# Performance work log

Measured on AMD Instinct MI355X. Metric: run time of the kernel, lower is better.

The kernel has to match this reference:

```python
import jax, jax.numpy as jnp
import numpy as np

N_NODES = 50000
N_EDGES = 800000
IN_CH, HID_CH, OUT_CH = 128, 128, 40


def setup_inputs() -> dict:
    key = jax.random.key(0)
    k1, k2, k3, k4 = jax.random.split(key, 4)
    x = jax.random.normal(k1, (N_NODES, IN_CH), dtype=jnp.float32)
    edge_index = jax.random.randint(k2, (2, N_EDGES), 0, N_NODES, dtype=jnp.int64)
    # Glorot-ish init for linear weights
    W1 = jax.random.normal(k3, (IN_CH, HID_CH), dtype=jnp.float32) / np.sqrt(IN_CH)
    b1 = jnp.zeros((HID_CH,), dtype=jnp.float32)
    W2 = jax.random.normal(k4, (HID_CH, OUT_CH), dtype=jnp.float32) / np.sqrt(HID_CH)
    b2 = jnp.zeros((OUT_CH,), dtype=jnp.float32)
    return {"x": x, "edge_index": edge_index, "W1": W1, "b1": b1, "W2": W2, "b2": b2}


def _gcn_conv(x, src, dst, W, b):
    # GCNConv(normalize=False): dense transform then sparse aggregation (scatter-add)
    h = x @ W                                   # [N, C_out]
    out = jax.ops.segment_sum(h[src], dst, num_segments=N_NODES)  # sum_{j->i} h[j]
    return out + b


def reference(x, edge_index, W1, b1, W2, b2):
    src, dst = edge_index[0], edge_index[1]
    h = _gcn_conv(x, src, dst, W1, b1)
    h = jax.nn.relu(h)
    # dropout is identity in eval mode
    h = _gcn_conv(h, src, dst, W2, b2)
    return jax.nn.log_softmax(h, axis=-1)
```

## Files before the change

kernel.cpp:

```cpp
#include <hip/hip_runtime.h>

#define NN 50000
#define NE 800000
#define NBKT 196
#define NBLK 256
#define EPB (NE / NBLK)
#define MATN (NBKT * NBLK)

using short8 = __attribute__((ext_vector_type(8))) short;
using f32x4  = __attribute__((ext_vector_type(4))) float;
union U4S8 { uint4 u; short8 v; };

__device__ __forceinline__ float lof(unsigned v) { return __uint_as_float(v << 16); }
__device__ __forceinline__ float hif(unsigned v) { return __uint_as_float(v & 0xffff0000u); }
__device__ __forceinline__ unsigned bf16rne(float f) {
    unsigned u = __float_as_uint(f);
    return (u + 0x7fffu + ((u >> 16) & 1u)) >> 16;
}
__device__ __forceinline__ unsigned pack2(float a, float b) {
    return bf16rne(a) | (bf16rne(b) << 16);
}
__device__ __forceinline__ unsigned fp8pack4(float a0, float a1, float a2, float a3) {
    int w = __builtin_amdgcn_cvt_pk_fp8_f32(a0, a1, 0, false);
    w = __builtin_amdgcn_cvt_pk_fp8_f32(a2, a3, w, true);
    return (unsigned)w;
}

__global__ __launch_bounds__(256) void binhist_k(const int* __restrict__ dst,
                                                 int* __restrict__ mat,
                                                 const float* __restrict__ W1,
                                                 const float* __restrict__ W2,
                                                 unsigned* __restrict__ W1T,
                                                 unsigned* __restrict__ W2T) {
    __shared__ int hist[NBKT];
    const int tid = threadIdx.x;
    for (int i = tid; i < NBKT; i += 256) hist[i] = 0;

    const int g = blockIdx.x * 256 + tid;
    if (g < 8192) {
        const int n = g >> 6, k2 = (g & 63) * 2;
        W1T[g] = pack2(W1[k2 * 128 + n], W1[(k2 + 1) * 128 + n]);
    } else if (g < 8192 + 3072) {
        const int u = g - 8192;
        const int n = u >> 6;
        const int q0 = (u & 63) * 2, q1 = q0 + 1;
        const int c0 = (q0 & 7) * 16 + (q0 >> 3);
        const int c1 = (q1 & 7) * 16 + (q1 >> 3);
        W2T[u] = (n < 40) ? pack2(W2[c0 * 40 + n], W2[c1 * 40 + n]) : 0u;
    }
    __syncthreads();

    const int base = blockIdx.x * EPB;
    for (int e = base + tid; e < base + EPB; e += 256)
        atomicAdd(&hist[dst[e] >> 8], 1);
    __syncthreads();
    for (int i = tid; i < NBKT; i += 256)
        mat[i * NBLK + blockIdx.x] = hist[i];
}

__global__ __launch_bounds__(256) void reduce_k(const int* __restrict__ mat,
                                                int* __restrict__ blocksum) {
    int v = mat[blockIdx.x * NBLK + threadIdx.x];
#pragma unroll
    for (int off = 32; off; off >>= 1) v += __shfl_xor(v, off, 64);
    __shared__ int ws[4];
    if ((threadIdx.x & 63) == 0) ws[threadIdx.x >> 6] = v;
    __syncthreads();
    if (threadIdx.x == 0) blocksum[blockIdx.x] = ws[0] + ws[1] + ws[2] + ws[3];
}

__global__ __launch_bounds__(256) void scanfin_k(int* __restrict__ mat,
                                                 const int* __restrict__ blocksum,
                                                 int* __restrict__ bucketoff) {
    __shared__ int bs[256];
    __shared__ int sm[256];
    const int t = threadIdx.x;
    const int b = blockIdx.x;
    const int mybs = (t < NBKT) ? blocksum[t] : 0;
    bs[t] = mybs;
    __syncthreads();
#pragma unroll
    for (int off = 1; off < 256; off <<= 1) {
        int u = (t >= off) ? bs[t - off] : 0;
        __syncthreads();
        bs[t] += u;
        __syncthreads();
    }
    if (b == 0) {
        if (t < NBKT) bucketoff[t] = bs[t] - mybs;
        if (t == 0) bucketoff[NBKT] = NE;
    }
    const int boff = bs[b] - blocksum[b];

    const int v = mat[b * NBLK + t];
    sm[t] = v;
    __syncthreads();
#pragma unroll
    for (int off = 1; off < 256; off <<= 1) {
        int u = (t >= off) ? sm[t - off] : 0;
        __syncthreads();
        sm[t] += u;
        __syncthreads();
    }
    mat[b * NBLK + t] = boff + sm[t] - v;
}

__global__ __launch_bounds__(256) void scatter_k(const int* __restrict__ src,
                                                 const int* __restrict__ dst,
                                                 const int* __restrict__ mat,
                                                 unsigned* __restrict__ binned) {
    __shared__ int cur[NBKT];
    const int tid = threadIdx.x;
    for (int i = tid; i < NBKT; i += 256) cur[i] = mat[i * NBLK + blockIdx.x];
    __syncthreads();
    const int base = blockIdx.x * EPB;
    for (int e = base + tid; e < base + EPB; e += 256) {
        const int d = dst[e];
        const int p = atomicAdd(&cur[d >> 8], 1);
        binned[p] = ((unsigned)(d & 255) << 16) | (unsigned)src[e];
    }
}

__global__ __launch_bounds__(256) void csrgemm1_k(const unsigned* __restrict__ binned,
                                                  const int* __restrict__ bucketoff,
                                                  int* __restrict__ rowoff,
                                                  unsigned short* __restrict__ eid,
                                                  const float* __restrict__ x,
                                                  const unsigned* __restrict__ W1T,
                                                  uint2* __restrict__ H1) {
    __shared__ int cnt[256];
    __shared__ int off[256];
    const int tid = threadIdx.x;
    if (blockIdx.x < NBKT) {
        const int b = blockIdx.x;
        const int beg = bucketoff[b];
        const int end = bucketoff[b + 1];
        cnt[tid] = 0;
        __syncthreads();
        for (int i = beg + tid; i < end; i += 256)
            atomicAdd(&cnt[(binned[i] >> 16) & 255u], 1);
        __syncthreads();
        const int v = cnt[tid];
        off[tid] = v;
        __syncthreads();
#pragma unroll
        for (int o = 1; o < 256; o <<= 1) {
            int u = (tid >= o) ? off[tid - o] : 0;
            __syncthreads();
            off[tid] += u;
            __syncthreads();
        }
        const int excl = off[tid] - v;
        const int node = b * 256 + tid;
        if (node <= NN) rowoff[node] = beg + excl;
        cnt[tid] = excl;
        __syncthreads();
        for (int i = beg + tid; i < end; i += 256) {
            const unsigned e = binned[i];
            const int p = atomicAdd(&cnt[(e >> 16) & 255u], 1);
            eid[beg + p] = (unsigned short)(e & 0xffffu);
        }
        return;
    }
    const int lane = tid & 63;
    const int cl = lane & 15;
    const int kh = lane >> 4;
    const int gw = ((blockIdx.x - NBKT) * 256 + tid) >> 6;

    short8 Bf[8][4];
#pragma unroll
    for (int c = 0; c < 8; ++c)
#pragma unroll
        for (int kc = 0; kc < 4; ++kc) {
            U4S8 tb;
            tb.u = *(const uint4*)(W1T + ((c * 16 + cl) * 128 + kc * 32 + kh * 8) / 2);
            Bf[c][kc] = tb.v;
        }

    for (int mt = gw; mt < 3125; mt += 1024) {
        const int r0 = mt * 16;
        const float* ap = x + (long)(r0 + cl) * 128 + kh * 8;
        f32x4 acc[8];
#pragma unroll
        for (int c = 0; c < 8; ++c) acc[c] = (f32x4){0.f, 0.f, 0.f, 0.f};
#pragma unroll
        for (int kc = 0; kc < 4; ++kc) {
            const float4 p0 = *(const float4*)(ap + kc * 32);
            const float4 p1 = *(const float4*)(ap + kc * 32 + 4);
            U4S8 af;
            af.u.x = pack2(p0.x, p0.y);
            af.u.y = pack2(p0.z, p0.w);
            af.u.z = pack2(p1.x, p1.y);
            af.u.w = pack2(p1.z, p1.w);
#pragma unroll
            for (int c = 0; c < 8; ++c)
                acc[c] = __builtin_amdgcn_mfma_f32_16x16x32_bf16(af.v, Bf[c][kc], acc[c], 0, 0, 0);
        }
#pragma unroll
        for (int j = 0; j < 4; ++j) {
            uint2 o;
            o.x = fp8pack4(acc[0][j], acc[1][j], acc[2][j], acc[3][j]);
            o.y = fp8pack4(acc[4][j], acc[5][j], acc[6][j], acc[7][j]);
            H1[(long)(r0 + kh * 4 + j) * 16 + cl] = o;
        }
    }
}

__global__ __launch_bounds__(256) void gather1_k(const uint4* __restrict__ H1,
                                                 const int* __restrict__ rowoff,
                                                 const unsigned short* __restrict__ eid,
                                                 const float* __restrict__ b1,
                                                 uint4* __restrict__ h) {
    const int n = blockIdx.x * 4 + (threadIdx.x >> 6);
    const int lane = threadIdx.x & 63;
    const int g = lane >> 3;
    const int cl = lane & 7;
    const int beg = rowoff[n], end = rowoff[n + 1];
    float a[16];
#pragma unroll
    for (int i = 0; i < 16; ++i) a[i] = 0.f;

#define ACC16(v)                                                             \
    {                                                                        \
        auto t0 = __builtin_amdgcn_cvt_pk_f32_fp8((int)(v).x, false);        \
        auto t1 = __builtin_amdgcn_cvt_pk_f32_fp8((int)(v).x, true);         \
        auto t2 = __builtin_amdgcn_cvt_pk_f32_fp8((int)(v).y, false);        \
        auto t3 = __builtin_amdgcn_cvt_pk_f32_fp8((int)(v).y, true);         \
        auto t4 = __builtin_amdgcn_cvt_pk_f32_fp8((int)(v).z, false);        \
        auto t5 = __builtin_amdgcn_cvt_pk_f32_fp8((int)(v).z, true);         \
        auto t6 = __builtin_amdgcn_cvt_pk_f32_fp8((int)(v).w, false);        \
        auto t7 = __builtin_amdgcn_cvt_pk_f32_fp8((int)(v).w, true);         \
        a[0] += t0[0];  a[1] += t0[1];  a[2] += t1[0];  a[3] += t1[1];       \
        a[4] += t2[0];  a[5] += t2[1];  a[6] += t3[0];  a[7] += t3[1];       \
        a[8] += t4[0];  a[9] += t4[1];  a[10] += t5[0]; a[11] += t5[1];      \
        a[12] += t6[0]; a[13] += t6[1]; a[14] += t7[0]; a[15] += t7[1];      \
    }

    int k = beg;
    for (; k + 15 < end; k += 16) {
        const uint4 vA = H1[eid[k + g] * 8 + cl];
        const uint4 vB = H1[eid[k + 8 + g] * 8 + cl];
        ACC16(vA);
        ACC16(vB);
    }
    for (; k + 7 < end; k += 8) {
        const uint4 v = H1[eid[k + g] * 8 + cl];
        ACC16(v);
    }
    if (k + g < end) {
        const uint4 v = H1[eid[k + g] * 8 + cl];
        ACC16(v);
    }
#undef ACC16

#pragma unroll
    for (int i = 0; i < 16; ++i) {
        a[i] += __shfl_xor(a[i], 8, 64);
        a[i] += __shfl_xor(a[i], 16, 64);
        a[i] += __shfl_xor(a[i], 32, 64);
    }
    if (lane < 8) {
        float r[16];
#pragma unroll
        for (int i = 0; i < 16; ++i)
            r[i] = fmaxf(a[i] + b1[(i & 7) * 16 + cl * 2 + (i >> 3)], 0.f);
        uint4 o1, o2;
        o1.x = pack2(r[0], r[1]);  o1.y = pack2(r[2], r[3]);
        o1.z = pack2(r[4], r[5]);  o1.w = pack2(r[6], r[7]);
        o2.x = pack2(r[8], r[9]);  o2.y = pack2(r[10], r[11]);
        o2.z = pack2(r[12], r[13]); o2.w = pack2(r[14], r[15]);
        h[n * 16 + cl * 2] = o1;
        h[n * 16 + cl * 2 + 1] = o2;
    }
}

__global__ __launch_bounds__(256) void gemm2_k(const unsigned* __restrict__ h,
                                               const unsigned* __restrict__ W2T,
                                               unsigned short* __restrict__ H2) {
    const int lane = threadIdx.x & 63;
    const int cl = lane & 15;
    const int kh = lane >> 4;
    const int gw = (blockIdx.x * 256 + threadIdx.x) >> 6;

    short8 Bf[3][4];
#pragma unroll
    for (int c = 0; c < 3; ++c)
#pragma unroll
        for (int kc = 0; kc < 4; ++kc) {
            U4S8 tb;
            tb.u = *(const uint4*)(W2T + ((c * 16 + cl) * 128 + kc * 32 + kh * 8) / 2);
            Bf[c][kc] = tb.v;
        }

    for (int mt = gw; mt < 3125; mt += 1024) {
        const int r0 = mt * 16;
        const unsigned* ap = h + (long)(r0 + cl) * 64 + kh * 4;
        f32x4 acc[3];
#pragma unroll
        for (int c = 0; c < 3; ++c) acc[c] = (f32x4){0.f, 0.f, 0.f, 0.f};
#pragma unroll
        for (int kc = 0; kc < 4; ++kc) {
            U4S8 af;
            af.u = *(const uint4*)(ap + kc * 16);
#pragma unroll
            for (int c = 0; c < 3; ++c)
                acc[c] = __builtin_amdgcn_mfma_f32_16x16x32_bf16(af.v, Bf[c][kc], acc[c], 0, 0, 0);
        }
        unsigned short* hp = H2 + (long)(r0 + kh * 4) * 64;
#pragma unroll
        for (int c = 0; c < 3; ++c) {
            const int col = c * 16 + cl;
            if (col < 40) {
#pragma unroll
                for (int j = 0; j < 4; ++j)
                    hp[j * 64 + col] = (unsigned short)bf16rne(acc[c][j]);
            }
        }
    }
}

__global__ __launch_bounds__(256) void gather2_k(const uint2* __restrict__ H2,
                                                 const int* __restrict__ rowoff,
                                                 const unsigned short* __restrict__ eid,
                                                 const float* __restrict__ b2,
                                                 float* __restrict__ out) {
    const int n = blockIdx.x * 4 + (threadIdx.x >> 6);
    const int lane = threadIdx.x & 63;
    const int g = lane / 10;
    const int c2 = lane - g * 10;
    const int beg = rowoff[n], end = rowoff[n + 1];
    float ax = 0.f, ay = 0.f, az = 0.f, aw = 0.f;
    if (g < 6) {
        int k = beg + g;
        for (; k + 6 < end; k += 12) {
            const uint2 v0 = H2[eid[k] * 16 + c2];
            const uint2 v1 = H2[eid[k + 6] * 16 + c2];
            ax += lof(v0.x) + lof(v1.x);
            ay += hif(v0.x) + hif(v1.x);
            az += lof(v0.y) + lof(v1.y);
            aw += hif(v0.y) + hif(v1.y);
        }
        if (k < end) {
            const uint2 v = H2[eid[k] * 16 + c2];
            ax += lof(v.x); ay += hif(v.x);
            az += lof(v.y); aw += hif(v.y);
        }
    }
    ax += __shfl(ax, lane + 30, 64); ay += __shfl(ay, lane + 30, 64);
    az += __shfl(az, lane + 30, 64); aw += __shfl(aw, lane + 30, 64);
    ax += __shfl(ax, lane + 10, 64) + __shfl(ax, lane + 20, 64);
    ay += __shfl(ay, lane + 10, 64) + __shfl(ay, lane + 20, 64);
    az += __shfl(az, lane + 10, 64) + __shfl(az, lane + 20, 64);
    aw += __shfl(aw, lane + 10, 64) + __shfl(aw, lane + 20, 64);

    const bool act = (lane < 10);
    float4 b = {0.f, 0.f, 0.f, 0.f};
    if (act) b = ((const float4*)b2)[lane];
    const float vx = ax + b.x, vy = ay + b.y, vz = az + b.z, vw = aw + b.w;
    float m = act ? fmaxf(fmaxf(vx, vy), fmaxf(vz, vw)) : -INFINITY;
#pragma unroll
    for (int off = 32; off; off >>= 1) m = fmaxf(m, __shfl_xor(m, off, 64));
    float e = act ? (expf(vx - m) + expf(vy - m) + expf(vz - m) + expf(vw - m)) : 0.f;
#pragma unroll
    for (int off = 32; off; off >>= 1) e += __shfl_xor(e, off, 64);
    const float ls = logf(e);
    if (act) {
        float4 o = {vx - m - ls, vy - m - ls, vz - m - ls, vw - m - ls};
        ((float4*)(out + (long)n * 40))[lane] = o;
    }
}

extern "C" void kernel_launch(void* const* d_in, const int* in_sizes, int n_in,
                              void* d_out, int out_size, void* d_ws, size_t ws_size,
                              hipStream_t stream) {
    const float* x  = (const float*)d_in[0];
    const int*   ei = (const int*)d_in[1];
    const float* W1 = (const float*)d_in[2];
    const float* b1 = (const float*)d_in[3];
    const float* W2 = (const float*)d_in[4];
    const float* b2 = (const float*)d_in[5];
    const int* src = ei;
    const int* dst = ei + NE;

    unsigned* H1   = (unsigned*)d_ws;
    unsigned* h    = H1 + (size_t)NN * 32;
    unsigned* H2   = h + (size_t)NN * 64;
    unsigned* W1T  = H2 + (size_t)NN * 32;
    unsigned* W2T  = W1T + 8192;
    int* mat       = (int*)(W2T + 3072);
    int* blocksum  = mat + MATN;
    int* bucketoff = blocksum + 256;
    int* rowoff    = bucketoff + NBKT + 1;
    unsigned short* eid = (unsigned short*)(rowoff + NN + 1);
    unsigned* binned = h;
    float* out     = (float*)d_out;

    binhist_k<<<NBLK, 256, 0, stream>>>(dst, mat, W1, W2, W1T, W2T);
    reduce_k<<<NBKT, 256, 0, stream>>>(mat, blocksum);
    scanfin_k<<<NBKT, 256, 0, stream>>>(mat, blocksum, bucketoff);
    scatter_k<<<NBLK, 256, 0, stream>>>(src, dst, mat, binned);
    csrgemm1_k<<<NBKT + 256, 256, 0, stream>>>(binned, bucketoff, rowoff, eid,
                                               x, W1T, (uint2*)H1);
    gather1_k<<<12500, 256, 0, stream>>>((const uint4*)H1, rowoff, eid, b1, (uint4*)h);
    gemm2_k<<<256, 256, 0, stream>>>(h, W2T, (unsigned short*)H2);
    gather2_k<<<12500, 256, 0, stream>>>((const uint2*)H2, rowoff, eid, b2, out);
}
```

Before: 106.2 us.

## Fuse histogram scan into scatter kernel and widen layer-2 gather loads

```diff
diff --git a/kernel.cpp b/kernel.cpp
--- a/kernel.cpp
+++ b/kernel.cpp
@@ -58,62 +58,53 @@
         mat[i * NBLK + blockIdx.x] = hist[i];
 }
 
-__global__ __launch_bounds__(256) void reduce_k(const int* __restrict__ mat,
-                                                int* __restrict__ blocksum) {
-    int v = mat[blockIdx.x * NBLK + threadIdx.x];
-#pragma unroll
-    for (int off = 32; off; off >>= 1) v += __shfl_xor(v, off, 64);
-    __shared__ int ws[4];
-    if ((threadIdx.x & 63) == 0) ws[threadIdx.x >> 6] = v;
+__global__ __launch_bounds__(256) void scanscatter_k(const int* __restrict__ src,
+                                                     const int* __restrict__ dst,
+                                                     const int* __restrict__ mat,
+                                                     unsigned* __restrict__ binned,
+                                                     int* __restrict__ bucketoff) {
+    __shared__ int tot[NBKT];
+    __shared__ int cur[NBKT];
+    __shared__ int sc[256];
+    const int tid = threadIdx.x;
+    const int lane = tid & 63;
+    const int w = tid >> 6;
+    const int b = blockIdx.x;
+    for (int i = w; i < NBKT; i += 4) {
+        int t = 0, p = 0;
+#pragma unroll
+        for (int c = 0; c < 4; ++c) {
+            const int col = c * 64 + lane;
+            const int v = mat[i * NBLK + col];
+            t += v;
+            p += (col < b) ? v : 0;
+        }
+#pragma unroll
+        for (int off = 32; off; off >>= 1) {
+            t += __shfl_xor(t, off, 64);
+            p += __shfl_xor(p, off, 64);
+        }
+        if (lane == 0) { tot[i] = t; cur[i] = p; }
+    }
     __syncthreads();
-    if (threadIdx.x == 0) blocksum[blockIdx.x] = ws[0] + ws[1] + ws[2] + ws[3];
-}
-
-__global__ __launch_bounds__(256) void scanfin_k(int* __restrict__ mat,
-                                                 const int* __restrict__ blocksum,
-                                                 int* __restrict__ bucketoff) {
-    __shared__ int bs[256];
-    __shared__ int sm[256];
-    const int t = threadIdx.x;
-    const int b = blockIdx.x;
-    const int mybs = (t < NBKT) ? blocksum[t] : 0;
-    bs[t] = mybs;
+    const int v = (tid < NBKT) ? tot[tid] : 0;
+    sc[tid] = v;
     __syncthreads();
 #pragma unroll
     for (int off = 1; off < 256; off <<= 1) {
-        int u = (t >= off) ? bs[t - off] : 0;
-        __syncthreads();
-        bs[t] += u;
-        __syncthreads();
-    }
+        int u = (tid >= off) ? sc[tid - off] : 0;
+        __syncthreads();
+        sc[tid] += u;
+        __syncthreads();
+    }
+    const int excl = sc[tid] - v;
+    if (tid < NBKT) cur[tid] += excl;
     if (b == 0) {
-        if (t < NBKT) bucketoff[t] = bs[t] - mybs;
-        if (t == 0) bucketoff[NBKT] = NE;
-    }
-    const int boff = bs[b] - blocksum[b];
-
-    const int v = mat[b * NBLK + t];
-    sm[t] = v;
+        if (tid < NBKT) bucketoff[tid] = excl;
+        if (tid == 0) bucketoff[NBKT] = NE;
+    }
     __syncthreads();
-#pragma unroll
-    for (int off = 1; off < 256; off <<= 1) {
-        int u = (t >= off) ? sm[t - off] : 0;
-        __syncthreads();
-        sm[t] += u;
-        __syncthreads();
-    }
-    mat[b * NBLK + t] = boff + sm[t] - v;
-}
-
-__global__ __launch_bounds__(256) void scatter_k(const int* __restrict__ src,
-                                                 const int* __restrict__ dst,
-                                                 const int* __restrict__ mat,
-                                                 unsigned* __restrict__ binned) {
-    __shared__ int cur[NBKT];
-    const int tid = threadIdx.x;
-    for (int i = tid; i < NBKT; i += 256) cur[i] = mat[i * NBLK + blockIdx.x];
-    __syncthreads();
-    const int base = blockIdx.x * EPB;
+    const int base = b * EPB;
     for (int e = base + tid; e < base + EPB; e += 256) {
         const int d = dst[e];
         const int p = atomicAdd(&cur[d >> 8], 1);
@@ -319,54 +310,69 @@
     }
 }
 
-__global__ __launch_bounds__(256) void gather2_k(const uint2* __restrict__ H2,
+__global__ __launch_bounds__(256) void gather2_k(const uint4* __restrict__ H2,
                                                  const int* __restrict__ rowoff,
                                                  const unsigned short* __restrict__ eid,
                                                  const float* __restrict__ b2,
                                                  float* __restrict__ out) {
     const int n = blockIdx.x * 4 + (threadIdx.x >> 6);
     const int lane = threadIdx.x & 63;
-    const int g = lane / 10;
-    const int c2 = lane - g * 10;
+    const int g = lane / 5;
+    const int c4 = lane - g * 5;
     const int beg = rowoff[n], end = rowoff[n + 1];
-    float ax = 0.f, ay = 0.f, az = 0.f, aw = 0.f;
-    if (g < 6) {
+    float a0 = 0.f, a1 = 0.f, a2 = 0.f, a3 = 0.f, a4 = 0.f, a5 = 0.f, a6 = 0.f, a7 = 0.f;
+    if (g < 12) {
         int k = beg + g;
-        for (; k + 6 < end; k += 12) {
-            const uint2 v0 = H2[eid[k] * 16 + c2];
-            const uint2 v1 = H2[eid[k + 6] * 16 + c2];
-            ax += lof(v0.x) + lof(v1.x);
-            ay += hif(v0.x) + hif(v1.x);
-            az += lof(v0.y) + lof(v1.y);
-            aw += hif(v0.y) + hif(v1.y);
+        for (; k + 12 < end; k += 24) {
+            const uint4 v0 = H2[eid[k] * 8 + c4];
+            const uint4 v1 = H2[eid[k + 12] * 8 + c4];
+            a0 += lof(v0.x) + lof(v1.x); a1 += hif(v0.x) + hif(v1.x);
+            a2 += lof(v0.y) + lof(v1.y); a3 += hif(v0.y) + hif(v1.y);
+            a4 += lof(v0.z) + lof(v1.z); a5 += hif(v0.z) + hif(v1.z);
+            a6 += lof(v0.w) + lof(v1.w); a7 += hif(v0.w) + hif(v1.w);
         }
         if (k < end) {
-            const uint2 v = H2[eid[k] * 16 + c2];
-            ax += lof(v.x); ay += hif(v.x);
-            az += lof(v.y); aw += hif(v.y);
-        }
-    }
-    ax += __shfl(ax, lane + 30, 64); ay += __shfl(ay, lane + 30, 64);
-    az += __shfl(az, lane + 30, 64); aw += __shfl(aw, lane + 30, 64);
-    ax += __shfl(ax, lane + 10, 64) + __shfl(ax, lane + 20, 64);
-    ay += __shfl(ay, lane + 10, 64) + __shfl(ay, lane + 20, 64);
-    az += __shfl(az, lane + 10, 64) + __shfl(az, lane + 20, 64);
-    aw += __shfl(aw, lane + 10, 64) + __shfl(aw, lane + 20, 64);
-
-    const bool act = (lane < 10);
-    float4 b = {0.f, 0.f, 0.f, 0.f};
-    if (act) b = ((const float4*)b2)[lane];
-    const float vx = ax + b.x, vy = ay + b.y, vz = az + b.z, vw = aw + b.w;
-    float m = act ? fmaxf(fmaxf(vx, vy), fmaxf(vz, vw)) : -INFINITY;
+            const uint4 v = H2[eid[k] * 8 + c4];
+            a0 += lof(v.x); a1 += hif(v.x);
+            a2 += lof(v.y); a3 += hif(v.y);
+            a4 += lof(v.z); a5 += hif(v.z);
+            a6 += lof(v.w); a7 += hif(v.w);
+        }
+    }
+#define FOLD1(A, D) A += __shfl(A, lane + (D), 64)
+#define FOLD2(A) A += __shfl(A, lane + 5, 64) + __shfl(A, lane + 10, 64)
+    FOLD1(a0, 30); FOLD1(a1, 30); FOLD1(a2, 30); FOLD1(a3, 30);
+    FOLD1(a4, 30); FOLD1(a5, 30); FOLD1(a6, 30); FOLD1(a7, 30);
+    FOLD1(a0, 15); FOLD1(a1, 15); FOLD1(a2, 15); FOLD1(a3, 15);
+    FOLD1(a4, 15); FOLD1(a5, 15); FOLD1(a6, 15); FOLD1(a7, 15);
+    FOLD2(a0); FOLD2(a1); FOLD2(a2); FOLD2(a3);
+    FOLD2(a4); FOLD2(a5); FOLD2(a6); FOLD2(a7);
+#undef FOLD1
+#undef FOLD2
+
+    const bool act = (lane < 5);
+    float4 bA = {0.f, 0.f, 0.f, 0.f}, bB = {0.f, 0.f, 0.f, 0.f};
+    if (act) {
+        bA = ((const float4*)b2)[lane * 2];
+        bB = ((const float4*)b2)[lane * 2 + 1];
+    }
+    const float v0 = a0 + bA.x, v1 = a1 + bA.y, v2 = a2 + bA.z, v3 = a3 + bA.w;
+    const float v4 = a4 + bB.x, v5 = a5 + bB.y, v6 = a6 + bB.z, v7 = a7 + bB.w;
+    float m = act ? fmaxf(fmaxf(fmaxf(v0, v1), fmaxf(v2, v3)),
+                          fmaxf(fmaxf(v4, v5), fmaxf(v6, v7))) : -INFINITY;
 #pragma unroll
     for (int off = 32; off; off >>= 1) m = fmaxf(m, __shfl_xor(m, off, 64));
-    float e = act ? (expf(vx - m) + expf(vy - m) + expf(vz - m) + expf(vw - m)) : 0.f;
+    float e = act ? (expf(v0 - m) + expf(v1 - m) + expf(v2 - m) + expf(v3 - m) +
+                     expf(v4 - m) + expf(v5 - m) + expf(v6 - m) + expf(v7 - m)) : 0.f;
 #pragma unroll
     for (int off = 32; off; off >>= 1) e += __shfl_xor(e, off, 64);
     const float ls = logf(e);
     if (act) {
-        float4 o = {vx - m - ls, vy - m - ls, vz - m - ls, vw - m - ls};
-        ((float4*)(out + (long)n * 40))[lane] = o;
+        float4 oA = {v0 - m - ls, v1 - m - ls, v2 - m - ls, v3 - m - ls};
+        float4 oB = {v4 - m - ls, v5 - m - ls, v6 - m - ls, v7 - m - ls};
+        float4* op = (float4*)(out + (long)n * 40 + lane * 8);
+        op[0] = oA;
+        op[1] = oB;
     }
 }
 
@@ -388,20 +394,17 @@
     unsigned* W1T  = H2 + (size_t)NN * 32;
     unsigned* W2T  = W1T + 8192;
     int* mat       = (int*)(W2T + 3072);
-    int* blocksum  = mat + MATN;
-    int* bucketoff = blocksum + 256;
+    int* bucketoff = mat + MATN;
     int* rowoff    = bucketoff + NBKT + 1;
     unsigned short* eid = (unsigned short*)(rowoff + NN + 1);
     unsigned* binned = h;
     float* out     = (float*)d_out;
 
     binhist_k<<<NBLK, 256, 0, stream>>>(dst, mat, W1, W2, W1T, W2T);
-    reduce_k<<<NBKT, 256, 0, stream>>>(mat, blocksum);
-    scanfin_k<<<NBKT, 256, 0, stream>>>(mat, blocksum, bucketoff);
-    scatter_k<<<NBLK, 256, 0, stream>>>(src, dst, mat, binned);
+    scanscatter_k<<<NBLK, 256, 0, stream>>>(src, dst, mat, binned, bucketoff);
     csrgemm1_k<<<NBKT + 256, 256, 0, stream>>>(binned, bucketoff, rowoff, eid,
                                                x, W1T, (uint2*)H1);
     gather1_k<<<12500, 256, 0, stream>>>((const uint4*)H1, rowoff, eid, b1, (uint4*)h);
     gemm2_k<<<256, 256, 0, stream>>>(h, W2T, (unsigned short*)H2);
-    gather2_k<<<12500, 256, 0, stream>>>((const uint2*)H2, rowoff, eid, b2, out);
-}
+    gather2_k<<<12500, 256, 0, stream>>>((const uint4*)H2, rowoff, eid, b2, out);
+}
```

Result: slower. 129.4 us (+21.8%).

## Store layer-2 features in FP8 and regather with 16-lane column layout

Applied to the files above, without the earlier changes.

```diff
diff --git a/kernel.cpp b/kernel.cpp
--- a/kernel.cpp
+++ b/kernel.cpp
@@ -276,7 +276,7 @@
 
 __global__ __launch_bounds__(256) void gemm2_k(const unsigned* __restrict__ h,
                                                const unsigned* __restrict__ W2T,
-                                               unsigned short* __restrict__ H2) {
+                                               unsigned* __restrict__ H2) {
     const int lane = threadIdx.x & 63;
     const int cl = lane & 15;
     const int kh = lane >> 4;
@@ -306,67 +306,69 @@
             for (int c = 0; c < 3; ++c)
                 acc[c] = __builtin_amdgcn_mfma_f32_16x16x32_bf16(af.v, Bf[c][kc], acc[c], 0, 0, 0);
         }
-        unsigned short* hp = H2 + (long)(r0 + kh * 4) * 64;
-#pragma unroll
-        for (int c = 0; c < 3; ++c) {
-            const int col = c * 16 + cl;
-            if (col < 40) {
-#pragma unroll
-                for (int j = 0; j < 4; ++j)
-                    hp[j * 64 + col] = (unsigned short)bf16rne(acc[c][j]);
-            }
-        }
-    }
-}
-
-__global__ __launch_bounds__(256) void gather2_k(const uint2* __restrict__ H2,
+#pragma unroll
+        for (int j = 0; j < 4; ++j)
+            H2[(long)(r0 + kh * 4 + j) * 16 + cl] =
+                fp8pack4(acc[0][j], acc[1][j], acc[2][j], 0.f);
+    }
+}
+
+__global__ __launch_bounds__(256) void gather2_k(const unsigned* __restrict__ H2,
                                                  const int* __restrict__ rowoff,
                                                  const unsigned short* __restrict__ eid,
                                                  const float* __restrict__ b2,
                                                  float* __restrict__ out) {
     const int n = blockIdx.x * 4 + (threadIdx.x >> 6);
     const int lane = threadIdx.x & 63;
-    const int g = lane / 10;
-    const int c2 = lane - g * 10;
+    const int g = lane >> 4;
+    const int q = lane & 15;
     const int beg = rowoff[n], end = rowoff[n + 1];
-    float ax = 0.f, ay = 0.f, az = 0.f, aw = 0.f;
-    if (g < 6) {
-        int k = beg + g;
-        for (; k + 6 < end; k += 12) {
-            const uint2 v0 = H2[eid[k] * 16 + c2];
-            const uint2 v1 = H2[eid[k + 6] * 16 + c2];
-            ax += lof(v0.x) + lof(v1.x);
-            ay += hif(v0.x) + hif(v1.x);
-            az += lof(v0.y) + lof(v1.y);
-            aw += hif(v0.y) + hif(v1.y);
-        }
-        if (k < end) {
-            const uint2 v = H2[eid[k] * 16 + c2];
-            ax += lof(v.x); ay += hif(v.x);
-            az += lof(v.y); aw += hif(v.y);
-        }
-    }
-    ax += __shfl(ax, lane + 30, 64); ay += __shfl(ay, lane + 30, 64);
-    az += __shfl(az, lane + 30, 64); aw += __shfl(aw, lane + 30, 64);
-    ax += __shfl(ax, lane + 10, 64) + __shfl(ax, lane + 20, 64);
-    ay += __shfl(ay, lane + 10, 64) + __shfl(ay, lane + 20, 64);
-    az += __shfl(az, lane + 10, 64) + __shfl(az, lane + 20, 64);
-    aw += __shfl(aw, lane + 10, 64) + __shfl(aw, lane + 20, 64);
-
-    const bool act = (lane < 10);
-    float4 b = {0.f, 0.f, 0.f, 0.f};
-    if (act) b = ((const float4*)b2)[lane];
-    const float vx = ax + b.x, vy = ay + b.y, vz = az + b.z, vw = aw + b.w;
-    float m = act ? fmaxf(fmaxf(vx, vy), fmaxf(vz, vw)) : -INFINITY;
-#pragma unroll
-    for (int off = 32; off; off >>= 1) m = fmaxf(m, __shfl_xor(m, off, 64));
-    float e = act ? (expf(vx - m) + expf(vy - m) + expf(vz - m) + expf(vw - m)) : 0.f;
-#pragma unroll
-    for (int off = 32; off; off >>= 1) e += __shfl_xor(e, off, 64);
+    float a0 = 0.f, a1 = 0.f, a2 = 0.f;
+
+#define ACCQ(u)                                                              \
+    {                                                                        \
+        auto t0 = __builtin_amdgcn_cvt_pk_f32_fp8((int)(u), false);          \
+        auto t1 = __builtin_amdgcn_cvt_pk_f32_fp8((int)(u), true);           \
+        a0 += t0[0]; a1 += t0[1]; a2 += t1[0];                               \
+    }
+
+    int k = beg;
+    for (; k + 7 < end; k += 8) {
+        const unsigned uA = H2[eid[k + g] * 16 + q];
+        const unsigned uB = H2[eid[k + 4 + g] * 16 + q];
+        ACCQ(uA);
+        ACCQ(uB);
+    }
+    for (; k + 3 < end; k += 4) {
+        const unsigned u = H2[eid[k + g] * 16 + q];
+        ACCQ(u);
+    }
+    if (k + g < end) {
+        const unsigned u = H2[eid[k + g] * 16 + q];
+        ACCQ(u);
+    }
+#undef ACCQ
+
+    a0 += __shfl_xor(a0, 16, 64); a0 += __shfl_xor(a0, 32, 64);
+    a1 += __shfl_xor(a1, 16, 64); a1 += __shfl_xor(a1, 32, 64);
+    a2 += __shfl_xor(a2, 16, 64); a2 += __shfl_xor(a2, 32, 64);
+
+    const bool has2 = (q < 8);
+    const float v0 = a0 + b2[q];
+    const float v1 = a1 + b2[16 + q];
+    const float v2 = has2 ? (a2 + b2[32 + q]) : -INFINITY;
+    float m = fmaxf(fmaxf(v0, v1), v2);
+#pragma unroll
+    for (int off = 8; off; off >>= 1) m = fmaxf(m, __shfl_xor(m, off, 64));
+    float e = expf(v0 - m) + expf(v1 - m) + (has2 ? expf(v2 - m) : 0.f);
+#pragma unroll
+    for (int off = 8; off; off >>= 1) e += __shfl_xor(e, off, 64);
     const float ls = logf(e);
-    if (act) {
-        float4 o = {vx - m - ls, vy - m - ls, vz - m - ls, vw - m - ls};
-        ((float4*)(out + (long)n * 40))[lane] = o;
+    if (lane < 16) {
+        float* op = out + (long)n * 40;
+        op[q] = v0 - m - ls;
+        op[16 + q] = v1 - m - ls;
+        if (has2) op[32 + q] = v2 - m - ls;
     }
 }
 
@@ -385,7 +387,7 @@
     unsigned* H1   = (unsigned*)d_ws;
     unsigned* h    = H1 + (size_t)NN * 32;
     unsigned* H2   = h + (size_t)NN * 64;
-    unsigned* W1T  = H2 + (size_t)NN * 32;
+    unsigned* W1T  = H2 + (size_t)NN * 16;
     unsigned* W2T  = W1T + 8192;
     int* mat       = (int*)(W2T + 3072);
     int* blocksum  = mat + MATN;
@@ -402,6 +404,6 @@
     csrgemm1_k<<<NBKT + 256, 256, 0, stream>>>(binned, bucketoff, rowoff, eid,
                                                x, W1T, (uint2*)H1);
     gather1_k<<<12500, 256, 0, stream>>>((const uint4*)H1, rowoff, eid, b1, (uint4*)h);
-    gemm2_k<<<256, 256, 0, stream>>>(h, W2T, (unsigned short*)H2);
-    gather2_k<<<12500, 256, 0, stream>>>((const uint2*)H2, rowoff, eid, b2, out);
-}
+    gemm2_k<<<256, 256, 0, stream>>>(h, W2T, H2);
+    gather2_k<<<12500, 256, 0, stream>>>(H2, rowoff, eid, b2, out);
+}
```

Result: faster. 103.7 us (-2.4%).
